# Performance work log

Hardware: AMD Instinct MI355X
Metric: run time of the kernel (lower is better)

Reference implementation:

```python
import jax, jax.numpy as jnp
import numpy as np
from jax import lax

EPS = 1e-5
INPLANES = 256


def setup_inputs() -> dict:
    key = jax.random.key(0)
    ks = jax.random.split(key, 7)
    C = INPLANES
    C2 = C // 2
    x = jax.random.normal(ks[0], (4, C, 128, 128), dtype=jnp.float32)
    s = 1.0 / np.sqrt(C)
    theta_w = jax.random.normal(ks[1], (C2, C), dtype=jnp.float32) * s
    phi_w = jax.random.normal(ks[2], (C2, C), dtype=jnp.float32) * s
    g_w = jax.random.normal(ks[3], (C2, C), dtype=jnp.float32) * s
    y_w = jax.random.normal(ks[4], (C, C2), dtype=jnp.float32) * (1.0 / np.sqrt(C2))
    bn_weight = jax.random.normal(ks[5], (C,), dtype=jnp.float32) * 0.1
    bn_bias = jax.random.normal(ks[6], (C,), dtype=jnp.float32) * 0.1
    return {"x": x, "theta_w": theta_w, "phi_w": phi_w, "g_w": g_w,
            "y_w": y_w, "bn_weight": bn_weight, "bn_bias": bn_bias}


def reference(x, theta_w, phi_w, g_w, y_w, bn_weight, bn_bias):
    # compression: per-channel 3x3 max pool, stride 2, VALID (matches
    # F.max_pool3d(kernel=(1,3,3), stride=(1,2,2)) on a 4D tensor)
    xp = lax.reduce_window(x, -jnp.inf, lax.max,
                           (1, 1, 3, 3), (1, 1, 2, 2), 'VALID')
    B, C, H, W = xp.shape
    C2 = C // 2
    N = H * W
    residual = xp
    # 1x1 convs are channel GEMMs
    theta = jnp.einsum('oc,bchw->bohw', theta_w, xp).reshape(B, C2, N)
    phi = jnp.einsum('oc,bchw->bohw', phi_w, xp).reshape(B, C2, N)
    g = jnp.einsum('oc,bchw->bohw', g_w, xp).reshape(B, C2, N)
    theta = jnp.transpose(theta, (0, 2, 1))  # (B, N, C2)
    g = jnp.transpose(g, (0, 2, 1))          # (B, N, C2)
    # embedded-gaussian attention: (B,N,N) scores, unscaled
    f = jax.nn.softmax(jnp.einsum('bnc,bcm->bnm', theta, phi), axis=-1)
    y = jnp.einsum('bnm,bmc->bnc', f, g)     # (B, N, C2)
    # FAITHFUL to torch: raw .view of contiguous (B,N,C2) into (B,C2,H,W)
    out = y.reshape(B, C2, H, W)
    out = jnp.einsum('oc,bchw->bohw', y_w, out)
    # BatchNorm2d, training mode (biased batch variance)
    mean = jnp.mean(out, axis=(0, 2, 3), keepdims=True)
    var = jnp.var(out, axis=(0, 2, 3), keepdims=True)
    out = (out - mean) * lax.rsqrt(var + EPS)
    out = out * bn_weight[None, :, None, None] + bn_bias[None, :, None, None]
    return jax.nn.relu(out + residual)
```

## Files before the change

### kernel.cpp

```cpp
#include <hip/hip_runtime.h>

#define B_   4
#define C_   256
#define C2_  128
#define HIN  128
#define HO   63
#define NSEQ 3969
#define NPAD 4032
#define QPAD 4096
#define D_   128
#define TOT  (B_*C_*NSEQ)
#define SPLITS 3

typedef _Float16 f16x8 __attribute__((ext_vector_type(8)));
typedef short    s16x8 __attribute__((ext_vector_type(8)));
typedef float    f32x4 __attribute__((ext_vector_type(4)));
typedef unsigned short u16;
typedef u16 u16x8 __attribute__((ext_vector_type(8)));

#define MFMA16(a,b,c) __builtin_amdgcn_mfma_f32_16x16x32_f16((a),(b),(c),0,0,0)
#define MFMABF(a,b,c) __builtin_amdgcn_mfma_f32_16x16x32_bf16((a),(b),(c),0,0,0)

__device__ __forceinline__ float b2f(u16 u) {
  unsigned v = ((unsigned)u) << 16;
  return __builtin_bit_cast(float, v);
}
__device__ __forceinline__ u16 f2b(float f) {
  unsigned u = __builtin_bit_cast(unsigned, f);
  return (u16)((u + 0x7FFFu + ((u >> 16) & 1u)) >> 16);
}

template<int CTRL>
__device__ __forceinline__ float dppf(float x) {
  return __builtin_bit_cast(float,
      __builtin_amdgcn_mov_dpp(__builtin_bit_cast(int, x), CTRL, 0xF, 0xF, true));
}
__device__ __forceinline__ float rmax16(float x) {
  x = fmaxf(x, dppf<0xB1>(x));
  x = fmaxf(x, dppf<0x4E>(x));
  x = fmaxf(x, dppf<0x124>(x));
  x = fmaxf(x, dppf<0x128>(x));
  return x;
}
__device__ __forceinline__ float rsum16(float x) {
  x += dppf<0xB1>(x);
  x += dppf<0x4E>(x);
  x += dppf<0x124>(x);
  x += dppf<0x128>(x);
  return x;
}

__global__ __launch_bounds__(256) void pool_k(
    const float* __restrict__ x, float* __restrict__ xp, u16* __restrict__ xpT2,
    u16* __restrict__ W2, const float* __restrict__ tw, const float* __restrict__ pw,
    const float* __restrict__ gw, float* gsum, float* gsq) {
  __shared__ unsigned Tls[64 * 69];
  int h = blockIdx.x, cg = blockIdx.y, b = blockIdx.z;
  int tid = threadIdx.x;
  if (cg == 4) {
    if (h == 0 && b == 0) { gsum[tid] = 0.f; gsq[tid] = 0.f; }
    int base = ((b * 63 + h) * 256 + tid) * 2;
#pragma unroll
    for (int e2 = 0; e2 < 2; e2++) {
      int e = base + e2;
      if (e < 3 * 128 * 256) {
        int mat = e >> 15, idx = e & 32767;
        int oc = idx >> 8, k = idx & 255;
        const float* W = (mat == 0) ? tw : (mat == 1) ? pw : gw;
        float v = W[oc * 256 + k];
        u16 hi = f2b(v);
        u16 lo = f2b(v - b2f(hi));
        W2[((long)(mat * 128 + oc)) * 512 + 2 * k]     = hi;
        W2[((long)(mat * 128 + oc)) * 512 + 2 * k + 1] = lo;
      }
    }
    return;
  }
  int cl = tid >> 2, w0 = (tid & 3) << 4;
  int c = cg * 64 + cl;
  long rowbase = ((long)(b * C_ + c) * HIN + 2 * h) * HIN + 2 * w0;
  float best[16];
#pragma unroll
  for (int j = 0; j < 16; j++) best[j] = -3e38f;
#pragma unroll
  for (int dh = 0; dh < 3; dh++) {
    long ro = rowbase + dh * HIN;
    float v[40];
#pragma unroll
    for (int ch = 0; ch < 10; ch++) {
      f32x4 a = *(const f32x4*)(x + ro + ch * 4);
#pragma unroll
      for (int j = 0; j < 4; j++) v[ch * 4 + j] = a[j];
    }
#pragma unroll
    for (int j = 0; j < 16; j++)
      best[j] = fmaxf(best[j], fmaxf(fmaxf(v[2 * j], v[2 * j + 1]), v[2 * j + 2]));
  }
  long xo = (long)(b * C_ + c) * NPAD + h * HO + w0;
#pragma unroll
  for (int j = 0; j < 16; j++)
    if (w0 + j < HO) xp[xo + j] = best[j];
#pragma unroll
  for (int j = 0; j < 16; j++) {
    u16 hi = f2b(best[j]);
    u16 lo = f2b(best[j] - b2f(hi));
    Tls[cl * 69 + w0 + j] = (unsigned)hi | ((unsigned)lo << 16);
  }
  __syncthreads();
  int w = tid >> 2, cc0 = (tid & 3) << 4;
  if (w < HO) {
    int p = h * HO + w;
    u16 outv[32];
#pragma unroll
    for (int j = 0; j < 16; j++) {
      unsigned word = Tls[(cc0 + j) * 69 + w];
      outv[2 * j]     = (u16)(word & 0xFFFF);
      outv[2 * j + 1] = (u16)(word >> 16);
    }
    u16* d = xpT2 + ((long)b * NPAD + p) * 512 + 2 * (cg * 64 + cc0);
#pragma unroll
    for (int q = 0; q < 4; q++)
      *(u16x8*)(d + q * 8) = *(u16x8*)&outv[q * 8];
  }
}

__global__ __launch_bounds__(256) void qkv_k(
    const u16* __restrict__ xpT2, const u16* __restrict__ W2,
    _Float16* Qh, _Float16* Ql, _Float16* Kv, _Float16* Vt) {
  __shared__ u16 Asm[64 * 256];
  __shared__ u16 Bsm[64 * 256];
  __shared__ float Tsm[4][16][64];
  int pt = blockIdx.x, y = blockIdx.y, b = blockIdx.z;
  int tid = threadIdx.x, wave = tid >> 6, lane = tid & 63;
  int quad = lane >> 4, l16 = lane & 15;
  int mat = y >> 1, half = y & 1;
  const u16* Wr = W2 + ((long)(mat * 128 + half * 64)) * 512;
  const u16* Xb = xpT2 + ((long)b * NPAD + pt * 64) * 512;
  f32x4 acc[4];
#pragma unroll
  for (int s = 0; s < 4; s++) acc[s] = (f32x4){0.f, 0.f, 0.f, 0.f};
#pragma unroll
  for (int ck = 0; ck < 2; ck++) {
    if (ck) __syncthreads();
#pragma unroll
    for (int i = 0; i < 8; i++) {
      int g = tid + i * 256;
      int r = g >> 5, ccc = g & 31;
      int sw = (ccc ^ (r & 15)) << 3;
      *(u16x8*)&Asm[r * 256 + sw] = *(const u16x8*)(Wr + (long)r * 512 + ck * 256 + ccc * 8);
      *(u16x8*)&Bsm[r * 256 + sw] = *(const u16x8*)(Xb + (long)r * 512 + ck * 256 + ccc * 8);
    }
    __syncthreads();
#pragma unroll
    for (int kc = 0; kc < 8; kc++) {
      s16x8 a = *(const s16x8*)&Asm[(wave * 16 + l16) * 256 + (((kc * 4 + quad) ^ l16) << 3)];
#pragma unroll
      for (int s = 0; s < 4; s++) {
        s16x8 bv = *(const s16x8*)&Bsm[(s * 16 + l16) * 256 + (((kc * 4 + quad) ^ l16) << 3)];
        acc[s] = MFMABF(a, bv, acc[s]);
      }
    }
  }
  int chanb = half * 64 + wave * 16;
  if (mat == 2) {
    _Float16* dv = Vt + (long)b * C2_ * NPAD;
#pragma unroll
    for (int s = 0; s < 4; s++)
#pragma unroll
      for (int r = 0; r < 4; r++) {
        int p = pt * 64 + s * 16 + l16;
        if (p < NSEQ) dv[(long)(chanb + quad * 4 + r) * NPAD + p] = (_Float16)acc[s][r];
      }
  } else {
#pragma unroll
    for (int s = 0; s < 4; s++)
#pragma unroll
      for (int r = 0; r < 4; r++)
        Tsm[wave][quad * 4 + r][s * 16 + l16] = acc[s][r];
    int p = pt * 64 + lane;
    if (p < NSEQ) {
      f16x8 hv[2], lv[2];
#pragma unroll
      for (int cl2 = 0; cl2 < 16; cl2++) {
        float v = Tsm[wave][cl2][lane];
        _Float16 hx = (_Float16)v;
        hv[cl2 >> 3][cl2 & 7] = hx;
        lv[cl2 >> 3][cl2 & 7] = (_Float16)(v - (float)hx);
      }
      if (mat == 0) {
        _Float16* dh = Qh + ((long)b * QPAD + p) * 128 + chanb;
        _Float16* dl = Ql + ((long)b * QPAD + p) * 128 + chanb;
        *(f16x8*)dh = hv[0]; *(f16x8*)(dh + 8) = hv[1];
        *(f16x8*)dl = lv[0]; *(f16x8*)(dl + 8) = lv[1];
      } else {
        _Float16* dk = Kv + ((long)b * NPAD + p) * 128 + chanb;
        *(f16x8*)dk = hv[0]; *(f16x8*)(dk + 8) = hv[1];
      }
    }
  }
}

__global__ __launch_bounds__(256, 3) void flash_k(
    const _Float16* __restrict__ Qh, const _Float16* __restrict__ Ql,
    const _Float16* __restrict__ Kv, const _Float16* __restrict__ Vt,
    float* __restrict__ Opart, float* __restrict__ Mp, float* __restrict__ Lp) {
  __shared__ _Float16 Ks[64 * 128];
  __shared__ _Float16 Vs[128 * 64];
  __shared__ _Float16 Ps[4 * 1024];
  int qt = blockIdx.x, split = blockIdx.y, b = blockIdx.z;
  int tid = threadIdx.x, wave = tid >> 6, lane = tid & 63;
  int quad = lane >> 4, l16 = lane & 15;
  const _Float16* Qhb = Qh + (long)b * QPAD * D_;
  const _Float16* Qlb = Ql + (long)b * QPAD * D_;
  const _Float16* Kb  = Kv + (long)b * NPAD * D_;
  const _Float16* Vb  = Vt + (long)b * C2_ * NPAD;

  long qrow = qt * 64 + wave * 16 + l16;
  f16x8 aqh[4], aql[4];
#pragma unroll
  for (int kk = 0; kk < 4; kk++) {
    aqh[kk] = *(const f16x8*)(Qhb + qrow * D_ + kk * 32 + quad * 8);
    aql[kk] = *(const f16x8*)(Qlb + qrow * D_ + kk * 32 + quad * 8);
  }
  f32x4 o_acc[8];
#pragma unroll
  for (int s = 0; s < 8; s++) o_acc[s] = (f32x4){0.f, 0.f, 0.f, 0.f};
  float m_r[4] = {-3e38f, -3e38f, -3e38f, -3e38f};
  float l_r[4] = {0.f, 0.f, 0.f, 0.f};
  const float LOG2E = 1.4426950408889634f;
  int po = wave * 1024;
  int t0 = split * 21, t1 = t0 + 21;

  int rK = tid >> 4, qK = tid & 15;
  int cV = tid >> 3, qV = tid & 7;
  const _Float16* Kg = Kb + rK * D_ + qK * 8;
  const _Float16* Vg = Vb + (long)cV * NPAD + qV * 8;
  int lk = rK * 128 + ((qK ^ (rK & 15)) << 3);
  int lv = cV * 64 + ((qV ^ (cV & 7)) << 3);

  f16x8 pk0, pk1, pk2, pk3, pv0, pv1, pv2, pv3;
  {
    long ko = (long)t0 * 8192;
    pk0 = *(const f16x8*)(Kg + ko);
    pk1 = *(const f16x8*)(Kg + ko + 2048);
    pk2 = *(const f16x8*)(Kg + ko + 4096);
    pk3 = *(const f16x8*)(Kg + ko + 6144);
    int vo = t0 * 64;
    pv0 = *(const f16x8*)(Vg + vo);
    pv1 = *(const f16x8*)(Vg + vo + (long)32 * NPAD);
    pv2 = *(const f16x8*)(Vg + vo + (long)64 * NPAD);
    pv3 = *(const f16x8*)(Vg + vo + (long)96 * NPAD);
  }

#pragma unroll 1
  for (int t = t0; t < t1; t++) {
    __syncthreads();
    *(f16x8*)&Ks[lk]        = pk0;
    *(f16x8*)&Ks[lk + 2048] = pk1;
    *(f16x8*)&Ks[lk + 4096] = pk2;
    *(f16x8*)&Ks[lk + 6144] = pk3;
    *(f16x8*)&Vs[lv]        = pv0;
    *(f16x8*)&Vs[lv + 2048] = pv1;
    *(f16x8*)&Vs[lv + 4096] = pv2;
    *(f16x8*)&Vs[lv + 6144] = pv3;
    __syncthreads();
    if (t + 1 < t1) {
      long ko = (long)(t + 1) * 8192;
      pk0 = *(const f16x8*)(Kg + ko);
      pk1 = *(const f16x8*)(Kg + ko + 2048);
      pk2 = *(const f16x8*)(Kg + ko + 4096);
      pk3 = *(const f16x8*)(Kg + ko + 6144);
      int vo = (t + 1) * 64;
      pv0 = *(const f16x8*)(Vg + vo);
      pv1 = *(const f16x8*)(Vg + vo + (long)32 * NPAD);
      pv2 = *(const f16x8*)(Vg + vo + (long)64 * NPAD);
      pv3 = *(const f16x8*)(Vg + vo + (long)96 * NPAD);
    }

    f32x4 s_acc[4];
#pragma unroll
    for (int s = 0; s < 4; s++) s_acc[s] = (f32x4){0.f, 0.f, 0.f, 0.f};
    __builtin_amdgcn_s_setprio(1);
#pragma unroll
    for (int kk = 0; kk < 4; kk++) {
      f16x8 bh[4];
#pragma unroll
      for (int s = 0; s < 4; s++)
        bh[s] = *(const f16x8*)&Ks[(s * 16 + l16) * 128 + (((kk * 4 + quad) ^ l16) << 3)];
#pragma unroll
      for (int s = 0; s < 4; s++) s_acc[s] = MFMA16(aqh[kk], bh[s], s_acc[s]);
#pragma unroll
      for (int s = 0; s < 4; s++) s_acc[s] = MFMA16(aql[kk], bh[s], s_acc[s]);
    }
    __builtin_amdgcn_s_setprio(0);

#pragma unroll
    for (int s = 0; s < 4; s++) {
      if (t * 64 + s * 16 + l16 >= NSEQ) {
#pragma unroll
        for (int r = 0; r < 4; r++) s_acc[s][r] = -3e38f;
      }
    }
    float mx[4];
#pragma unroll
    for (int r = 0; r < 4; r++) {
      mx[r] = fmaxf(fmaxf(s_acc[0][r], s_acc[1][r]), fmaxf(s_acc[2][r], s_acc[3][r]));
      mx[r] = rmax16(mx[r]);
    }
    bool need = false;
#pragma unroll
    for (int r = 0; r < 4; r++) need = need || (mx[r] > m_r[r] + 8.0f);
    if (__any(need)) {
      float alpha[4];
#pragma unroll
      for (int r = 0; r < 4; r++) {
        float mn = fmaxf(m_r[r], mx[r]);
        alpha[r] = exp2f((m_r[r] - mn) * LOG2E);
        m_r[r] = mn;
        l_r[r] *= alpha[r];
      }
#pragma unroll
      for (int s8 = 0; s8 < 8; s8++)
#pragma unroll
        for (int r = 0; r < 4; r++) o_acc[s8][r] *= alpha[r];
    }
    float rs[4] = {0.f, 0.f, 0.f, 0.f};
#pragma unroll
    for (int s = 0; s < 4; s++)
#pragma unroll
      for (int r = 0; r < 4; r++) {
        float p = exp2f((s_acc[s][r] - m_r[r]) * LOG2E);
        rs[r] += p;
        int m = quad * 4 + r;
        Ps[po + m * 64 + (((s * 2 + (l16 >> 3)) ^ (m & 7)) << 3) + (l16 & 7)] =
            (_Float16)p;
      }
#pragma unroll
    for (int r = 0; r < 4; r++) {
      rs[r] = rsum16(rs[r]);
      l_r[r] += rs[r];
    }
    f16x8 ap[2];
#pragma unroll
    for (int kk2 = 0; kk2 < 2; kk2++)
      ap[kk2] = *(const f16x8*)&Ps[po + l16 * 64 + (((kk2 * 4 + quad) ^ (l16 & 7)) << 3)];
    __builtin_amdgcn_s_setprio(1);
#pragma unroll
    for (int kk2 = 0; kk2 < 2; kk2++)
#pragma unroll
      for (int s8 = 0; s8 < 8; s8++) {
        int c2 = s8 * 16 + l16;
        f16x8 bv = *(const f16x8*)&Vs[c2 * 64 + (((kk2 * 4 + quad) ^ (c2 & 7)) << 3)];
        o_acc[s8] = MFMA16(ap[kk2], bv, o_acc[s8]);
      }
    __builtin_amdgcn_s_setprio(0);
  }

  float* Ob = Opart + (long)(b * SPLITS + split) * NSEQ * D_;
  float* Mb = Mp + (long)(b * SPLITS + split) * NSEQ;
  float* Lb = Lp + (long)(b * SPLITS + split) * NSEQ;
#pragma unroll
  for (int r = 0; r < 4; r++) {
    int n = qt * 64 + wave * 16 + quad * 4 + r;
    if (n < NSEQ) {
#pragma unroll
      for (int s8 = 0; s8 < 8; s8++)
        Ob[(long)n * D_ + s8 * 16 + l16] = o_acc[s8][r];
      if (l16 == 0) { Mb[n] = m_r[r]; Lb[n] = l_r[r]; }
    }
  }
}

__global__ __launch_bounds__(256) void merge_k(const float* __restrict__ Opart,
                                               const float* __restrict__ Mp,
                                               const float* __restrict__ Lp,
                                               float* __restrict__ Y) {
  int row = blockIdx.x * 4 + (threadIdx.x >> 6);
  int lane = threadIdx.x & 63;
  int b = row / NSEQ, n = row - b * NSEQ;
  const float LOG2E = 1.4426950408889634f;
  float ms[SPLITS], m = -3e38f;
#pragma unroll
  for (int s = 0; s < SPLITS; s++) {
    ms[s] = Mp[(long)(b * SPLITS + s) * NSEQ + n];
    m = fmaxf(m, ms[s]);
  }
  float den = 0.f, a0 = 0.f, a1 = 0.f;
  int d = lane * 2;
#pragma unroll
  for (int s = 0; s < SPLITS; s++) {
    float w = exp2f((ms[s] - m) * LOG2E);
    den += Lp[(long)(b * SPLITS + s) * NSEQ + n] * w;
    const float* O = Opart + ((long)(b * SPLITS + s) * NSEQ + n) * D_ + d;
    a0 += w * O[0];
    a1 += w * O[1];
  }
  float inv = 1.f / den;
  float* Yo = Y + ((long)b * NSEQ + n) * D_ + d;
  Yo[0] = a0 * inv;
  Yo[1] = a1 * inv;
}

__global__ __launch_bounds__(256) void out_k(const float* __restrict__ Y,
                                             const float* __restrict__ yw, float* outp,
                                             float* gsum, float* gsumsq) {
  int b = blockIdx.z, ot = blockIdx.y, pb = blockIdx.x, tid = threadIdx.x;
  __shared__ float Wt[C2_][16];
  __shared__ float red[2][16][4];
#pragma unroll
  for (int i = 0; i < 8; i++) {
    int g = tid + i * 256;
    int r = g >> 7, c = g & 127;
    Wt[c][r] = yw[(ot * 16 + r) * C2_ + c];
  }
  __syncthreads();
  int p0 = pb * 512 + tid;
  const float* Yb = Y + (long)b * NSEQ * D_;
  bool val[2];
#pragma unroll
  for (int j = 0; j < 2; j++) val[j] = (p0 + j * 256) < NSEQ;
  float acc[16][2];
#pragma unroll
  for (int r = 0; r < 16; r++)
#pragma unroll
    for (int j = 0; j < 2; j++) acc[r][j] = 0.f;
  for (int c = 0; c < C2_; c++) {
    float xv[2];
#pragma unroll
    for (int j = 0; j < 2; j++) xv[j] = val[j] ? Yb[(long)c * NSEQ + p0 + j * 256] : 0.f;
#pragma unroll
    for (int r4 = 0; r4 < 4; r4++) {
      f32x4 w4 = *(const f32x4*)&Wt[c][r4 * 4];
#pragma unroll
      for (int rr = 0; rr < 4; rr++)
#pragma unroll
        for (int j = 0; j < 2; j++) acc[r4 * 4 + rr][j] += w4[rr] * xv[j];
    }
  }
  long ob = ((long)b * C_ + ot * 16) * NSEQ;
#pragma unroll
  for (int r = 0; r < 16; r++)
#pragma unroll
    for (int j = 0; j < 2; j++)
      if (val[j]) outp[ob + (long)r * NSEQ + p0 + j * 256] = acc[r][j];
  int wave = tid >> 6, lane = tid & 63;
#pragma unroll
  for (int r = 0; r < 16; r++) {
    float s = 0.f, q = 0.f;
#pragma unroll
    for (int j = 0; j < 2; j++) { s += acc[r][j]; q += acc[r][j] * acc[r][j]; }
#pragma unroll
    for (int off = 1; off < 64; off <<= 1) {
      s += __shfl_xor(s, off, 64);
      q += __shfl_xor(q, off, 64);
    }
    if (lane == 0) { red[0][r][wave] = s; red[1][r][wave] = q; }
  }
  __syncthreads();
  if (tid < 32) {
    int which = tid >> 4, r = tid & 15;
    float v = red[which][r][0] + red[which][r][1] + red[which][r][2] + red[which][r][3];
    atomicAdd((which ? gsumsq : gsum) + ot * 16 + r, v);
  }
}

__global__ __launch_bounds__(256) void bn_k(const float* __restrict__ outp,
                                            const float* gsum, const float* gsumsq,
                                            const float* __restrict__ bnw,
                                            const float* __restrict__ bnb,
                                            const float* __restrict__ xp, float* out) {
  int idx = blockIdx.x * 256 + threadIdx.x;
  if (idx >= TOT) return;
  int p = idx % NSEQ;
  int bc = idx / NSEQ;
  int c = bc & (C_ - 1);
  const float invn = 1.0f / (float)(B_ * NSEQ);
  float mean = gsum[c] * invn;
  float var = gsumsq[c] * invn - mean * mean;
  var = fmaxf(var, 0.f);
  float is = rsqrtf(var + 1e-5f);
  float v = (outp[idx] - mean) * is * bnw[c] + bnb[c] + xp[(long)bc * NPAD + p];
  out[idx] = fmaxf(v, 0.f);
}

extern "C" void kernel_launch(void* const* d_in, const int* in_sizes, int n_in,
                              void* d_out, int out_size, void* d_ws, size_t ws_size,
                              hipStream_t stream) {
  size_t off = 0;
  auto alloc = [&](size_t bytes) -> char* {
    char* p = (char*)d_ws + off;
    off += (bytes + 255) & ~(size_t)255;
    return p;
  };
  float*    xp   = (float*)alloc(sizeof(float) * (size_t)B_ * C_ * NPAD);
  u16*      xpT2 = (u16*)alloc(2 * (size_t)B_ * NPAD * 512);
  u16*      W2   = (u16*)alloc(2 * (size_t)3 * 128 * 512);
  _Float16* Qh   = (_Float16*)alloc(2 * (size_t)B_ * QPAD * D_);
  _Float16* Ql   = (_Float16*)alloc(2 * (size_t)B_ * QPAD * D_);
  _Float16* Kv   = (_Float16*)alloc(2 * (size_t)B_ * NPAD * D_);
  _Float16* Vt   = (_Float16*)alloc(2 * (size_t)B_ * C2_ * NPAD);
  float*    big  = (float*)alloc(sizeof(float) * (size_t)B_ * SPLITS * NSEQ * D_);
  float*    gsum = (float*)alloc(1024);
  float*    gsq  = (float*)alloc(1024);

  float* Mp = (float*)xpT2;
  float* Lp = Mp + (size_t)B_ * SPLITS * NSEQ;
  float* Yb = (float*)Qh;

  const float* xin = (const float*)d_in[0];
  pool_k<<<dim3(63, 5, B_), 256, 0, stream>>>(xin, xp, xpT2, W2,
                                              (const float*)d_in[1], (const float*)d_in[2],
                                              (const float*)d_in[3], gsum, gsq);
  qkv_k<<<dim3(63, 6, B_), 256, 0, stream>>>(xpT2, W2, Qh, Ql, Kv, Vt);
  flash_k<<<dim3(63, SPLITS, B_), 256, 0, stream>>>(Qh, Ql, Kv, Vt, big, Mp, Lp);
  merge_k<<<3969, 256, 0, stream>>>(big, Mp, Lp, Yb);
  out_k<<<dim3(8, 16, B_), 256, 0, stream>>>(Yb, (const float*)d_in[4], big, gsum, gsq);
  bn_k<<<(TOT + 255) / 256, 256, 0, stream>>>(big, gsum, gsq,
                                              (const float*)d_in[5], (const float*)d_in[6],
                                              xp, (float*)d_out);
}
```

Measured before the change: 287.2 us.

## Use split-f16 MFMA for output projection and raise flash split count

Rewrites the y_w output projection kernel to run on MFMA instructions. Both the weights and Y are split into f16 hi/lo pairs interleaved along K, so the hi*hi+lo*lo pairs approximate fp32 precision, and operands are staged in swizzled shared memory. This replaces the scalar FMA loop, and the BN partial sums now come from per-16-lane reductions with atomics. It also raises the flash attention KV split from 3 to 4, with occupancy 4 in launch_bounds, giving more blocks for parallelism at the cost of more partial outputs to merge. The big buffer was sized by SPLITS, so it grows accordingly. The cross terms of the hi/lo split are dropped, which slightly reduces precision.

```diff
diff --git a/kernel.cpp b/kernel.cpp
--- a/kernel.cpp
+++ b/kernel.cpp
@@ -10,7 +10,7 @@
 #define QPAD 4096
 #define D_   128
 #define TOT  (B_*C_*NSEQ)
-#define SPLITS 3
+#define SPLITS 4
 
 typedef _Float16 f16x8 __attribute__((ext_vector_type(8)));
 typedef short    s16x8 __attribute__((ext_vector_type(8)));
@@ -200,7 +200,7 @@
   }
 }
 
-__global__ __launch_bounds__(256, 3) void flash_k(
+__global__ __launch_bounds__(256, 4) void flash_k(
     const _Float16* __restrict__ Qh, const _Float16* __restrict__ Ql,
     const _Float16* __restrict__ Kv, const _Float16* __restrict__ Vt,
     float* __restrict__ Opart, float* __restrict__ Mp, float* __restrict__ Lp) {
@@ -229,7 +229,8 @@
   float l_r[4] = {0.f, 0.f, 0.f, 0.f};
   const float LOG2E = 1.4426950408889634f;
   int po = wave * 1024;
-  int t0 = split * 21, t1 = t0 + 21;
+  int t0 = split * 16;
+  int t1 = (t0 + 16 < 63) ? (t0 + 16) : 63;
 
   int rK = tid >> 4, qK = tid & 15;
   int cV = tid >> 3, qV = tid & 7;
@@ -404,63 +405,75 @@
 __global__ __launch_bounds__(256) void out_k(const float* __restrict__ Y,
                                              const float* __restrict__ yw, float* outp,
                                              float* gsum, float* gsumsq) {
-  int b = blockIdx.z, ot = blockIdx.y, pb = blockIdx.x, tid = threadIdx.x;
-  __shared__ float Wt[C2_][16];
-  __shared__ float red[2][16][4];
+  __shared__ u16 Asm2[64 * 256];
+  __shared__ u16 Bsm2[64 * 256];
+  int pt = blockIdx.x, ct = blockIdx.y, b = blockIdx.z;
+  int tid = threadIdx.x, wave = tid >> 6, lane = tid & 63;
+  int quad = lane >> 4, l16 = lane & 15;
+  const float* Yb = Y + (long)b * NSEQ * D_;
+  int p0 = pt * 64;
 #pragma unroll
   for (int i = 0; i < 8; i++) {
     int g = tid + i * 256;
-    int r = g >> 7, c = g & 127;
-    Wt[c][r] = yw[(ot * 16 + r) * C2_ + c];
+    int r = g >> 5, ccc = g & 31;
+    f32x4 w4 = *(const f32x4*)(yw + (ct * 64 + r) * C2_ + ccc * 4);
+    u16 tw2[8];
+#pragma unroll
+    for (int j = 0; j < 4; j++) {
+      _Float16 hx = (_Float16)w4[j];
+      _Float16 lx = (_Float16)(w4[j] - (float)hx);
+      tw2[2 * j]     = __builtin_bit_cast(u16, hx);
+      tw2[2 * j + 1] = __builtin_bit_cast(u16, lx);
+    }
+    *(u16x8*)&Asm2[r * 256 + ((ccc ^ (r & 15)) << 3)] = *(u16x8*)tw2;
+    int p = g & 63, c4 = g >> 6;
+    u16 ty[8];
+    bool ok = (p0 + p) < NSEQ;
+#pragma unroll
+    for (int j = 0; j < 4; j++) {
+      int c2 = c4 * 4 + j;
+      float v = ok ? Yb[(long)c2 * NSEQ + p0 + p] : 0.f;
+      _Float16 hx = (_Float16)v;
+      _Float16 lx = (_Float16)(v - (float)hx);
+      ty[2 * j]     = __builtin_bit_cast(u16, hx);
+      ty[2 * j + 1] = __builtin_bit_cast(u16, lx);
+    }
+    *(u16x8*)&Bsm2[p * 256 + ((c4 ^ (p & 15)) << 3)] = *(u16x8*)ty;
   }
   __syncthreads();
-  int p0 = pb * 512 + tid;
-  const float* Yb = Y + (long)b * NSEQ * D_;
-  bool val[2];
-#pragma unroll
-  for (int j = 0; j < 2; j++) val[j] = (p0 + j * 256) < NSEQ;
-  float acc[16][2];
-#pragma unroll
-  for (int r = 0; r < 16; r++)
-#pragma unroll
-    for (int j = 0; j < 2; j++) acc[r][j] = 0.f;
-  for (int c = 0; c < C2_; c++) {
-    float xv[2];
-#pragma unroll
-    for (int j = 0; j < 2; j++) xv[j] = val[j] ? Yb[(long)c * NSEQ + p0 + j * 256] : 0.f;
-#pragma unroll
-    for (int r4 = 0; r4 < 4; r4++) {
-      f32x4 w4 = *(const f32x4*)&Wt[c][r4 * 4];
-#pragma unroll
-      for (int rr = 0; rr < 4; rr++)
-#pragma unroll
-        for (int j = 0; j < 2; j++) acc[r4 * 4 + rr][j] += w4[rr] * xv[j];
-    }
-  }
-  long ob = ((long)b * C_ + ot * 16) * NSEQ;
-#pragma unroll
-  for (int r = 0; r < 16; r++)
-#pragma unroll
-    for (int j = 0; j < 2; j++)
-      if (val[j]) outp[ob + (long)r * NSEQ + p0 + j * 256] = acc[r][j];
-  int wave = tid >> 6, lane = tid & 63;
-#pragma unroll
-  for (int r = 0; r < 16; r++) {
-    float s = 0.f, q = 0.f;
-#pragma unroll
-    for (int j = 0; j < 2; j++) { s += acc[r][j]; q += acc[r][j] * acc[r][j]; }
-#pragma unroll
-    for (int off = 1; off < 64; off <<= 1) {
-      s += __shfl_xor(s, off, 64);
-      q += __shfl_xor(q, off, 64);
-    }
-    if (lane == 0) { red[0][r][wave] = s; red[1][r][wave] = q; }
-  }
-  __syncthreads();
-  if (tid < 32) {
-    int which = tid >> 4, r = tid & 15;
-    float v = red[which][r][0] + red[which][r][1] + red[which][r][2] + red[which][r][3];
-    atomicAdd((which ? gsumsq : gsum) + ot * 16 + r, v);
+  f32x4 acc[4];
+#pragma unroll
+  for (int s = 0; s < 4; s++) acc[s] = (f32x4){0.f, 0.f, 0.f, 0.f};
+#pragma unroll
+  for (int kc = 0; kc < 8; kc++) {
+    f16x8 a = *(const f16x8*)&Asm2[(wave * 16 + l16) * 256 + (((kc * 4 + quad) ^ l16) << 3)];
+#pragma unroll
+    for (int s = 0; s < 4; s++) {
+      f16x8 bv = *(const f16x8*)&Bsm2[(s * 16 + l16) * 256 + (((kc * 4 + quad) ^ l16) << 3)];
+      acc[s] = MFMA16(a, bv, acc[s]);
+    }
+  }
+  long ob = ((long)b * C_ + ct * 64 + wave * 16) * NSEQ;
+#pragma unroll
+  for (int r = 0; r < 4; r++) {
+    int row = quad * 4 + r;
+    float s1 = 0.f, s2 = 0.f;
+#pragma unroll
+    for (int s = 0; s < 4; s++) {
+      int p = p0 + s * 16 + l16;
+      float v = acc[s][r];
+      if (p < NSEQ) {
+        outp[ob + (long)row * NSEQ + p] = v;
+        s1 += v;
+        s2 += v * v;
+      }
+    }
+    s1 = rsum16(s1);
+    s2 = rsum16(s2);
+    if (l16 == 0) {
+      atomicAdd(gsum + ct * 64 + wave * 16 + row, s1);
+      atomicAdd(gsumsq + ct * 64 + wave * 16 + row, s2);
+    }
   }
 }
 
@@ -514,7 +527,7 @@
   qkv_k<<<dim3(63, 6, B_), 256, 0, stream>>>(xpT2, W2, Qh, Ql, Kv, Vt);
   flash_k<<<dim3(63, SPLITS, B_), 256, 0, stream>>>(Qh, Ql, Kv, Vt, big, Mp, Lp);
   merge_k<<<3969, 256, 0, stream>>>(big, Mp, Lp, Yb);
-  out_k<<<dim3(8, 16, B_), 256, 0, stream>>>(Yb, (const float*)d_in[4], big, gsum, gsq);
+  out_k<<<dim3(63, 4, B_), 256, 0, stream>>>(Yb, (const float*)d_in[4], big, gsum, gsq);
   bn_k<<<(TOT + 255) / 256, 256, 0, stream>>>(big, gsum, gsq,
                                               (const float*)d_in[5], (const float*)d_in[6],
                                               xp, (float*)d_out);
```

Measured after the change: 433.3 us. +50.9%, slower.
